# Optimization experiments

Measured on AMD Instinct MI355X. Metric: run time of the kernel, lower is better.

The kernel has to match this reference:

```python
import jax, jax.numpy as jnp
import numpy as np

N = 179  # hardcoded positional-bias size in the source module
LN_EPS = 1e-5

def _spec_attn_wghts(dtype=jnp.float32):
    i = jnp.arange(N)
    return (jnp.abs(i[None, :] - i[:, None]) / N).astype(dtype)  # [N, N]

def setup_inputs() -> dict:
    key = jax.random.key(0)
    ks = jax.random.split(key, 4)
    B, S, E = 128, 179, 1024
    x = jax.random.normal(ks[0], (B, S, E), dtype=jnp.float32)
    Wq = jax.random.normal(ks[1], (E, E), dtype=jnp.float32) * (E ** -0.5)
    Wk = jax.random.normal(ks[2], (E, E), dtype=jnp.float32) * (E ** -0.5)
    Wv = jax.random.normal(ks[3], (E, E), dtype=jnp.float32) * (E ** -0.5)
    gamma = jnp.ones((E,), dtype=jnp.float32)
    beta = jnp.zeros((E,), dtype=jnp.float32)
    return {"x": x, "Wq": Wq, "Wk": Wk, "Wv": Wv, "gamma": gamma, "beta": beta}

def reference(x, Wq, Wk, Wv, gamma, beta):
    B, S, E = x.shape
    H = 16
    D = E // H
    scale = E ** -0.5  # note: source scales by emb_size**-0.5, not head_dim
    # torch Linear(bias=False): y = x @ W.T
    q = (x @ Wq.T).reshape(B, S, H, D).transpose(0, 2, 1, 3)  # [B,H,S,D]
    k = (x @ Wk.T).reshape(B, S, H, D).transpose(0, 2, 1, 3)
    v = (x @ Wv.T).reshape(B, S, H, D).transpose(0, 2, 1, 3)
    w = _spec_attn_wghts(x.dtype)  # [S,S] multiplicative positional bias
    attn = jnp.einsum('bhqd,bhkd->bhqk', q, k) * scale * w
    attn = jax.nn.softmax(attn, axis=-1)
    out = jnp.einsum('bhqk,bhkd->bhqd', attn, v)  # [B,H,S,D]
    out = out.transpose(0, 2, 1, 3).reshape(B, S, E)
    # LayerNorm over last dim
    mu = jnp.mean(out, axis=-1, keepdims=True)
    var = jnp.var(out, axis=-1, keepdims=True)
    out = (out - mu) * jax.lax.rsqrt(var + LN_EPS) * gamma + beta
    return out
```

## Files before the change

### kernel.cpp

```cpp
#include <hip/hip_runtime.h>
#include <hip/hip_bf16.h>
#include <math.h>

#define S_LEN  179
#define M_TOT  22912
#define S_PAD  192

typedef __attribute__((ext_vector_type(8))) short short8;
typedef __attribute__((ext_vector_type(4))) float f32x4;
typedef __attribute__((ext_vector_type(4))) unsigned short ushort4v;

__device__ inline unsigned short f2bf(float f) {
    union { float f; unsigned int i; } v; v.f = f;
    unsigned int x = v.i;
    unsigned int r = x + 0x7FFFu + ((x >> 16) & 1u);
    return (unsigned short)(r >> 16);
}
__device__ inline int imin(int a, int b) { return a < b ? a : b; }

__device__ inline void gl_lds16(const unsigned short* g, unsigned short* l) {
    __builtin_amdgcn_global_load_lds(
        (const __attribute__((address_space(1))) unsigned int*)g,
        (__attribute__((address_space(3))) unsigned int*)l, 16, 0, 0);
}


#define XQUADS 5865472
#define WQUADS 262144
__global__ __launch_bounds__(256) void cast_all(
    const float* __restrict__ x,
    const float* __restrict__ Wq,
    const float* __restrict__ Wk,
    const float* __restrict__ Wv,
    unsigned short* __restrict__ xb,
    unsigned short* __restrict__ wb)
{
    const int t = blockIdx.x * 256 + threadIdx.x;
    const float* src;
    unsigned short* dst;
    size_t off;
    if (t < XQUADS) {
        src = x; dst = xb; off = (size_t)t * 4;
    } else {
        const int u = t - XQUADS;
        const int mat = u / WQUADS;
        src = (mat == 0) ? Wq : (mat == 1 ? Wk : Wv);
        dst = wb + (size_t)mat * 1048576;
        off = (size_t)(u - mat * WQUADS) * 4;
    }
    const float4 f = *(const float4*)(src + off);
    ushort4v o;
    o[0] = f2bf(f.x); o[1] = f2bf(f.y); o[2] = f2bf(f.z); o[3] = f2bf(f.w);
    *(ushort4v*)(dst + off) = o;
}

__global__ __launch_bounds__(256) void qkv_gemm2(
    const unsigned short* __restrict__ xb,
    const unsigned short* __restrict__ wb,
    unsigned short* __restrict__ qb,
    unsigned short* __restrict__ kb,
    unsigned short* __restrict__ vT)
{
    __shared__ __align__(16) unsigned short As[128 * 64];
    __shared__ __align__(16) unsigned short Bs[128 * 64];

    const int zi = blockIdx.z;
    const unsigned short* W = wb + (size_t)zi * 1048576;
    const int m0 = blockIdx.x * 128;
    const int n0 = blockIdx.y * 128;
    const int tid  = threadIdx.x;
    const int wave = tid >> 6;
    const int lane = tid & 63;
    const int ln   = lane & 15;
    const int quad = lane >> 4;
    const int wm = (wave & 1) * 64;
    const int wn = (wave >> 1) * 64;

    const int srow  = tid >> 3;
    const int pchunk = tid & 7;
    const int lchunk = pchunk ^ (srow & 7);
    const unsigned short* ag = xb + (size_t)(m0 + srow) * 1024 + lchunk * 8;
    const unsigned short* bg = W  + (size_t)(n0 + srow) * 1024 + lchunk * 8;
    unsigned short* al = &As[srow * 64 + pchunk * 8];
    unsigned short* bl = &Bs[srow * 64 + pchunk * 8];

    f32x4 acc[4][4];
    #pragma unroll
    for (int i = 0; i < 4; ++i)
        #pragma unroll
        for (int j = 0; j < 4; ++j) acc[i][j] = (f32x4){0.f, 0.f, 0.f, 0.f};

    for (int kt = 0; kt < 16; ++kt) {
        const int k0 = kt * 64;
        #pragma unroll
        for (int i = 0; i < 4; ++i) {
            gl_lds16(ag + (size_t)i * 32 * 1024 + k0, al + i * 32 * 64);
            gl_lds16(bg + (size_t)i * 32 * 1024 + k0, bl + i * 32 * 64);
        }
        __syncthreads();
        #pragma unroll
        for (int kh = 0; kh < 2; ++kh) {
            short8 af[4], bf_[4];
            #pragma unroll
            for (int mi = 0; mi < 4; ++mi) {
                const int row = wm + mi * 16 + ln;
                const int pc  = (kh * 4 + quad) ^ (ln & 7);
                af[mi] = *(const short8*)&As[row * 64 + pc * 8];
            }
            #pragma unroll
            for (int ni = 0; ni < 4; ++ni) {
                const int row = wn + ni * 16 + ln;
                const int pc  = (kh * 4 + quad) ^ (ln & 7);
                bf_[ni] = *(const short8*)&Bs[row * 64 + pc * 8];
            }
            #pragma unroll
            for (int mi = 0; mi < 4; ++mi)
                #pragma unroll
                for (int ni = 0; ni < 4; ++ni)
                    acc[mi][ni] = __builtin_amdgcn_mfma_f32_16x16x32_bf16(af[mi], bf_[ni], acc[mi][ni], 0, 0, 0);
        }
        __syncthreads();
    }

    if (zi < 2) {
        unsigned short* out = (zi == 0) ? qb : kb;
        #pragma unroll
        for (int mi = 0; mi < 4; ++mi)
            #pragma unroll
            for (int ni = 0; ni < 4; ++ni) {
                const int col = n0 + wn + ni * 16 + ln;
                #pragma unroll
                for (int r = 0; r < 4; ++r) {
                    const int row = m0 + wm + mi * 16 + quad * 4 + r;
                    out[(size_t)row * 1024 + col] = f2bf(acc[mi][ni][r]);
                }
            }
    } else {
        #pragma unroll
        for (int mi = 0; mi < 4; ++mi)
            #pragma unroll
            for (int ni = 0; ni < 4; ++ni) {
                const int col = n0 + wn + ni * 16 + ln;
                const int h = col >> 6, d = col & 63;
                #pragma unroll
                for (int r = 0; r < 4; ++r) {
                    const int row = m0 + wm + mi * 16 + quad * 4 + r;
                    const int b = row / 179;
                    const int s = row - b * 179;
                    vT[(((size_t)b * 16 + h) * 64 + d) * S_PAD + s] = f2bf(acc[mi][ni][r]);
                }
            }
    }
}

__global__ void vt_pad_zero(unsigned short* __restrict__ vT)
{
    const int idx = blockIdx.x * 256 + threadIdx.x;
    const int row = idx >> 4;
    const int j   = idx & 15;
    if (j < 13)
        vT[(size_t)row * S_PAD + 179 + j] = 0;
}

__global__ __launch_bounds__(256) void attn2(
    const unsigned short* __restrict__ qb,
    const unsigned short* __restrict__ kb,
    const unsigned short* __restrict__ vT,
    float* __restrict__ out)
{
    __shared__ unsigned short pbuf[4][16][208];

    const int bh   = blockIdx.x;
    const int b    = bh >> 4;
    const int h    = bh & 15;
    const int qt   = blockIdx.y;
    const int wave = threadIdx.x >> 6;
    const int lane = threadIdx.x & 63;
    const int ln   = lane & 15;
    const int quad = lane >> 4;
    const int qs   = qt * 64 + wave * 16;
    const size_t mrow = (size_t)b * S_LEN;

    f32x4 sc[12];
    #pragma unroll
    for (int i = 0; i < 12; ++i) sc[i] = (f32x4){0.f, 0.f, 0.f, 0.f};

    const int qoff = imin(qs + ln, S_LEN - 1);
    const unsigned short* qrow = qb + (mrow + qoff) * 1024 + h * 64 + quad * 8;
    const short8 a0 = *(const short8*)(qrow);
    const short8 a1 = *(const short8*)(qrow + 32);
    #pragma unroll
    for (int nt = 0; nt < 12; ++nt) {
        const int koffr = imin(nt * 16 + ln, S_LEN - 1);
        const unsigned short* krow = kb + (mrow + koffr) * 1024 + h * 64 + quad * 8;
        const short8 b0 = *(const short8*)(krow);
        const short8 b1 = *(const short8*)(krow + 32);
        sc[nt] = __builtin_amdgcn_mfma_f32_16x16x32_bf16(a0, b0, sc[nt], 0, 0, 0);
        sc[nt] = __builtin_amdgcn_mfma_f32_16x16x32_bf16(a1, b1, sc[nt], 0, 0, 0);
    }

    const float CW = 1.0f / (179.0f * 32.0f);
    float mx[4] = {-INFINITY, -INFINITY, -INFINITY, -INFINITY};
    #pragma unroll
    for (int nt = 0; nt < 12; ++nt) {
        const int k = nt * 16 + ln;
        #pragma unroll
        for (int r = 0; r < 4; ++r) {
            const int q = qs + quad * 4 + r;
            float v;
            if (k < S_LEN) {
                int d = q - k; if (d < 0) d = -d;
                v = sc[nt][r] * ((float)d * CW);
            } else {
                v = -INFINITY;
            }
            sc[nt][r] = v;
            mx[r] = fmaxf(mx[r], v);
        }
    }
    #pragma unroll
    for (int r = 0; r < 4; ++r) {
        float m = mx[r];
        m = fmaxf(m, __shfl_xor(m, 1));
        m = fmaxf(m, __shfl_xor(m, 2));
        m = fmaxf(m, __shfl_xor(m, 4));
        m = fmaxf(m, __shfl_xor(m, 8));
        mx[r] = m;
    }
    float sum[4] = {0.f, 0.f, 0.f, 0.f};
    #pragma unroll
    for (int nt = 0; nt < 12; ++nt)
        #pragma unroll
        for (int r = 0; r < 4; ++r) {
            const float e = __expf(sc[nt][r] - mx[r]);
            sc[nt][r] = e;
            sum[r] += e;
        }
    #pragma unroll
    for (int r = 0; r < 4; ++r) {
        float s = sum[r];
        s += __shfl_xor(s, 1);
        s += __shfl_xor(s, 2);
        s += __shfl_xor(s, 4);
        s += __shfl_xor(s, 8);
        sum[r] = 1.0f / s;
    }

    #pragma unroll
    for (int nt = 0; nt < 12; ++nt)
        #pragma unroll
        for (int r = 0; r < 4; ++r)
            pbuf[wave][quad * 4 + r][nt * 16 + ln] = f2bf(sc[nt][r] * sum[r]);

    f32x4 o[4];
    #pragma unroll
    for (int i = 0; i < 4; ++i) o[i] = (f32x4){0.f, 0.f, 0.f, 0.f};
    const unsigned short* vbase = vT + (size_t)bh * 64 * S_PAD;
    #pragma unroll
    for (int kt = 0; kt < 6; ++kt) {
        const short8 pa = *(const short8*)&pbuf[wave][ln][kt * 32 + quad * 8];
        #pragma unroll
        for (int n2 = 0; n2 < 4; ++n2) {
            const short8 vb = *(const short8*)(vbase + (size_t)(n2 * 16 + ln) * S_PAD + kt * 32 + quad * 8);
            o[n2] = __builtin_amdgcn_mfma_f32_16x16x32_bf16(pa, vb, o[n2], 0, 0, 0);
        }
    }

    #pragma unroll
    for (int n2 = 0; n2 < 4; ++n2) {
        const int col = h * 64 + n2 * 16 + ln;
        #pragma unroll
        for (int r = 0; r < 4; ++r) {
            const int q = qs + quad * 4 + r;
            if (q < S_LEN)
                out[(mrow + q) * 1024 + col] = o[n2][r];
        }
    }
}

__device__ inline short8 ldcvt8(const float* p) {
    const float4 f0 = *(const float4*)p;
    const float4 f1 = *(const float4*)(p + 4);
    short8 r;
    r[0] = (short)(__float_as_uint(f0.x) >> 16); r[1] = (short)(__float_as_uint(f0.y) >> 16);
    r[2] = (short)(__float_as_uint(f0.z) >> 16); r[3] = (short)(__float_as_uint(f0.w) >> 16);
    r[4] = (short)(__float_as_uint(f1.x) >> 16); r[5] = (short)(__float_as_uint(f1.y) >> 16);
    r[6] = (short)(__float_as_uint(f1.z) >> 16); r[7] = (short)(__float_as_uint(f1.w) >> 16);
    return r;
}

__device__ inline void proj48(const float* __restrict__ xb,
                              const float* __restrict__ Wm,
                              int h, int wave, int quad, int ln,
                              f32x4 (&acc)[3][4])
{
    #pragma unroll
    for (int t = 0; t < 3; ++t)
        #pragma unroll
        for (int nt = 0; nt < 4; ++nt) acc[t][nt] = (f32x4){0.f, 0.f, 0.f, 0.f};

    const float* wr[4];
    #pragma unroll
    for (int nt = 0; nt < 4; ++nt)
        wr[nt] = Wm + (size_t)(h * 64 + nt * 16 + ln) * 1024;
    const float* xr[3];
    #pragma unroll
    for (int t = 0; t < 3; ++t) {
        int q = wave * 16 + 64 * t + ln;
        if (q > S_LEN - 1) q = S_LEN - 1;
        xr[t] = xb + (size_t)q * 1024;
    }
    for (int kk = 0; kk < 32; ++kk) {
        const int k0 = kk * 32 + quad * 8;
        short8 bfr[4];
        #pragma unroll
        for (int nt = 0; nt < 4; ++nt) bfr[nt] = ldcvt8(wr[nt] + k0);
        short8 af[3];
        #pragma unroll
        for (int t = 0; t < 3; ++t) af[t] = ldcvt8(xr[t] + k0);
        #pragma unroll
        for (int t = 0; t < 3; ++t)
            #pragma unroll
            for (int nt = 0; nt < 4; ++nt)
                acc[t][nt] = __builtin_amdgcn_mfma_f32_16x16x32_bf16(af[t], bfr[nt], acc[t][nt], 0, 0, 0);
    }
}

__global__ __launch_bounds__(256) void fused_attn(
    const float* __restrict__ x,
    const float* __restrict__ Wq,
    const float* __restrict__ Wk,
    const float* __restrict__ Wv,
    float* __restrict__ out)
{
    __shared__ __align__(16) unsigned short Ks[192 * 72];
    __shared__ __align__(16) unsigned short Vt[64 * 200];
    __shared__ __align__(16) unsigned short WScr[4][16 * 72];

    const int bh   = blockIdx.x;
    const int b    = bh >> 4;
    const int h    = bh & 15;
    const int wave = threadIdx.x >> 6;
    const int lane = threadIdx.x & 63;
    const int ln   = lane & 15;
    const int quad = lane >> 4;
    const float* xb = x + (size_t)b * S_LEN * 1024;

    f32x4 acc[3][4];
    short8 qa[3][2];
    unsigned short* scr = &WScr[wave][0];

    proj48(xb, Wq, h, wave, quad, ln, acc);
    #pragma unroll
    for (int t = 0; t < 3; ++t) {
        #pragma unroll
        for (int nt = 0; nt < 4; ++nt)
            #pragma unroll
            for (int r = 0; r < 4; ++r)
                scr[(quad * 4 + r) * 72 + nt * 16 + ln] = f2bf(acc[t][nt][r]);
        qa[t][0] = *(const short8*)&scr[ln * 72 + quad * 8];
        qa[t][1] = *(const short8*)&scr[ln * 72 + 32 + quad * 8];
    }

    proj48(xb, Wk, h, wave, quad, ln, acc);
    #pragma unroll
    for (int t = 0; t < 3; ++t)
        #pragma unroll
        for (int nt = 0; nt < 4; ++nt)
            #pragma unroll
            for (int r = 0; r < 4; ++r)
                Ks[(wave * 16 + 64 * t + quad * 4 + r) * 72 + nt * 16 + ln] = f2bf(acc[t][nt][r]);

    proj48(xb, Wv, h, wave, quad, ln, acc);
    #pragma unroll
    for (int t = 0; t < 3; ++t)
        #pragma unroll
        for (int nt = 0; nt < 4; ++nt)
            #pragma unroll
            for (int r = 0; r < 4; ++r)
                Vt[(nt * 16 + ln) * 200 + wave * 16 + 64 * t + quad * 4 + r] = f2bf(acc[t][nt][r]);

    __syncthreads();

    const float CW = 1.0f / (179.0f * 32.0f);
    #pragma unroll 1
    for (int t = 0; t < 3; ++t) {
        const int q0 = wave * 16 + 64 * t;

        f32x4 sc[12];
        #pragma unroll
        for (int i = 0; i < 12; ++i) sc[i] = (f32x4){0.f, 0.f, 0.f, 0.f};
        #pragma unroll
        for (int nt = 0; nt < 12; ++nt) {
            const short8 kb0 = *(const short8*)&Ks[(nt * 16 + ln) * 72 + quad * 8];
            const short8 kb1 = *(const short8*)&Ks[(nt * 16 + ln) * 72 + 32 + quad * 8];
            sc[nt] = __builtin_amdgcn_mfma_f32_16x16x32_bf16(qa[t][0], kb0, sc[nt], 0, 0, 0);
            sc[nt] = __builtin_amdgcn_mfma_f32_16x16x32_bf16(qa[t][1], kb1, sc[nt], 0, 0, 0);
        }

        float mx[4] = {-INFINITY, -INFINITY, -INFINITY, -INFINITY};
        #pragma unroll
        for (int nt = 0; nt < 12; ++nt) {
            const int k = nt * 16 + ln;
            #pragma unroll
            for (int r = 0; r < 4; ++r) {
                const int q = q0 + quad * 4 + r;
                float v;
                if (k < S_LEN) {
                    int d = q - k; if (d < 0) d = -d;
                    v = sc[nt][r] * ((float)d * CW);
                } else {
                    v = -INFINITY;
                }
                sc[nt][r] = v;
                mx[r] = fmaxf(mx[r], v);
            }
        }
        #pragma unroll
        for (int r = 0; r < 4; ++r) {
            float m = mx[r];
            m = fmaxf(m, __shfl_xor(m, 1));
            m = fmaxf(m, __shfl_xor(m, 2));
            m = fmaxf(m, __shfl_xor(m, 4));
            m = fmaxf(m, __shfl_xor(m, 8));
            mx[r] = m;
        }
        float sum[4] = {0.f, 0.f, 0.f, 0.f};
        #pragma unroll
        for (int nt = 0; nt < 12; ++nt)
            #pragma unroll
            for (int r = 0; r < 4; ++r) {
                const float e = __expf(sc[nt][r] - mx[r]);
                sc[nt][r] = e;
                sum[r] += e;
            }
        #pragma unroll
        for (int r = 0; r < 4; ++r) {
            float s = sum[r];
            s += __shfl_xor(s, 1);
            s += __shfl_xor(s, 2);
            s += __shfl_xor(s, 4);
            s += __shfl_xor(s, 8);
            sum[r] = 1.0f / s;
        }

        f32x4 o[4];
        #pragma unroll
        for (int i = 0; i < 4; ++i) o[i] = (f32x4){0.f, 0.f, 0.f, 0.f};
        #pragma unroll
        for (int kt = 0; kt < 6; ++kt) {
            #pragma unroll
            for (int c = 0; c < 2; ++c) {
                const int nt = kt * 2 + c;
                #pragma unroll
                for (int r = 0; r < 4; ++r)
                    scr[(quad * 4 + r) * 40 + c * 16 + ln] = f2bf(sc[nt][r] * sum[r]);
            }
            const short8 pa = *(const short8*)&scr[ln * 40 + quad * 8];
            #pragma unroll
            for (int n2 = 0; n2 < 4; ++n2) {
                const short8 vb = *(const short8*)&Vt[(n2 * 16 + ln) * 200 + kt * 32 + quad * 8];
                o[n2] = __builtin_amdgcn_mfma_f32_16x16x32_bf16(pa, vb, o[n2], 0, 0, 0);
            }
        }

        #pragma unroll
        for (int n2 = 0; n2 < 4; ++n2) {
            const int col = h * 64 + n2 * 16 + ln;
            #pragma unroll
            for (int r = 0; r < 4; ++r) {
                const int q = q0 + quad * 4 + r;
                if (q < S_LEN)
                    out[((size_t)b * S_LEN + q) * 1024 + col] = o[n2][r];
            }
        }
    }
}

__global__ __launch_bounds__(256) void ln_kernel(
    float* __restrict__ io,
    const float* __restrict__ g,
    const float* __restrict__ be)
{
    __shared__ float red[8];
    const int row = blockIdx.x;
    const int tid = threadIdx.x;
    float* p = io + (size_t)row * 1024 + tid * 4;

    const float4 u = *(const float4*)p;
    float v[4] = {u.x, u.y, u.z, u.w};
    float sum = 0.f, sq = 0.f;
    #pragma unroll
    for (int j = 0; j < 4; ++j) {
        sum += v[j];
        sq  += v[j] * v[j];
    }
    #pragma unroll
    for (int off = 1; off < 64; off <<= 1) {
        sum += __shfl_xor(sum, off);
        sq  += __shfl_xor(sq, off);
    }
    const int wv = tid >> 6, lane = tid & 63;
    if (lane == 0) { red[wv] = sum; red[4 + wv] = sq; }
    __syncthreads();
    sum = red[0] + red[1] + red[2] + red[3];
    sq  = red[4] + red[5] + red[6] + red[7];
    const float mean = sum * (1.0f / 1024.0f);
    const float var  = fmaxf(sq * (1.0f / 1024.0f) - mean * mean, 0.0f);
    const float inv  = rsqrtf(var + 1e-5f);
    const float4 gg = *(const float4*)(g + tid * 4);
    const float4 bb = *(const float4*)(be + tid * 4);
    float4 o;
    o.x = (v[0] - mean) * inv * gg.x + bb.x;
    o.y = (v[1] - mean) * inv * gg.y + bb.y;
    o.z = (v[2] - mean) * inv * gg.z + bb.z;
    o.w = (v[3] - mean) * inv * gg.w + bb.w;
    *(float4*)p = o;
}

extern "C" void kernel_launch(void* const* d_in, const int* in_sizes, int n_in,
                              void* d_out, int out_size, void* d_ws, size_t ws_size,
                              hipStream_t stream)
{
    const float* x     = (const float*)d_in[0];
    const float* Wq    = (const float*)d_in[1];
    const float* Wk    = (const float*)d_in[2];
    const float* Wv    = (const float*)d_in[3];
    const float* gamma = (const float*)d_in[4];
    const float* beta  = (const float*)d_in[5];
    float* out = (float*)d_out;

    const size_t XB  = (size_t)M_TOT * 1024 * 2;
    const size_t WBB = (size_t)3 * 1048576 * 2;
    const size_t QBB = XB, KBB = XB;
    const size_t VTB = (size_t)2048 * 64 * S_PAD * 2;
    const size_t NEED = XB + WBB + QBB + KBB + VTB;

    if (ws_size >= NEED) {
        char* ws = (char*)d_ws;
        unsigned short* xb = (unsigned short*)(ws);
        unsigned short* wb = (unsigned short*)(ws + XB);
        unsigned short* qb = (unsigned short*)(ws + XB + WBB);
        unsigned short* kb = (unsigned short*)(ws + XB + WBB + QBB);
        unsigned short* vT = (unsigned short*)(ws + XB + WBB + QBB + KBB);

        cast_all<<<25984, 256, 0, stream>>>(x, Wq, Wk, Wv, xb, wb);
        qkv_gemm2<<<dim3(179, 8, 3), 256, 0, stream>>>(xb, wb, qb, kb, vT);
        vt_pad_zero<<<8192, 256, 0, stream>>>(vT);
        attn2<<<dim3(2048, 3), 256, 0, stream>>>(qb, kb, vT, out);
        ln_kernel<<<M_TOT, 256, 0, stream>>>(out, gamma, beta);
    } else {
        fused_attn<<<2048, 256, 0, stream>>>(x, Wq, Wk, Wv, out);
        ln_kernel<<<M_TOT, 256, 0, stream>>>(out, gamma, beta);
    }
}
```

Baseline: 592.1 us.

## Stage K and V in LDS once per head and loop over query tiles

The attention kernel now launches one block per (batch, head) instead of three. Each block loads that head's K and V^T into padded shared memory once, then loops over three 64-row query tiles and reads K and V from LDS rather than global memory. The probability staging buffer shrinks to a per-wave 16x32 scratch that is filled one k-chunk at a time before each PV MFMA. This removes redundant global loads of K and V across query tiles, at the cost of fewer blocks (less parallelism), more LDS per block, and serialised query tiles within each block.

```diff
diff --git a/kernel.cpp b/kernel.cpp
--- a/kernel.cpp
+++ b/kernel.cpp
@@ -162,118 +162,147 @@
         vT[(size_t)row * S_PAD + 179 + j] = 0;
 }
 
-__global__ __launch_bounds__(256) void attn2(
+__global__ __launch_bounds__(256) void attn3(
     const unsigned short* __restrict__ qb,
     const unsigned short* __restrict__ kb,
     const unsigned short* __restrict__ vT,
     float* __restrict__ out)
 {
-    __shared__ unsigned short pbuf[4][16][208];
+    __shared__ __align__(16) unsigned short Ks[192 * 72];
+    __shared__ __align__(16) unsigned short Vs[64 * 200];
+    __shared__ __align__(16) unsigned short Ps[4][16 * 40];
 
     const int bh   = blockIdx.x;
     const int b    = bh >> 4;
     const int h    = bh & 15;
-    const int qt   = blockIdx.y;
-    const int wave = threadIdx.x >> 6;
-    const int lane = threadIdx.x & 63;
+    const int tid  = threadIdx.x;
+    const int wave = tid >> 6;
+    const int lane = tid & 63;
     const int ln   = lane & 15;
     const int quad = lane >> 4;
-    const int qs   = qt * 64 + wave * 16;
     const size_t mrow = (size_t)b * S_LEN;
-
-    f32x4 sc[12];
-    #pragma unroll
-    for (int i = 0; i < 12; ++i) sc[i] = (f32x4){0.f, 0.f, 0.f, 0.f};
-
-    const int qoff = imin(qs + ln, S_LEN - 1);
-    const unsigned short* qrow = qb + (mrow + qoff) * 1024 + h * 64 + quad * 8;
-    const short8 a0 = *(const short8*)(qrow);
-    const short8 a1 = *(const short8*)(qrow + 32);
-    #pragma unroll
-    for (int nt = 0; nt < 12; ++nt) {
-        const int koffr = imin(nt * 16 + ln, S_LEN - 1);
-        const unsigned short* krow = kb + (mrow + koffr) * 1024 + h * 64 + quad * 8;
-        const short8 b0 = *(const short8*)(krow);
-        const short8 b1 = *(const short8*)(krow + 32);
-        sc[nt] = __builtin_amdgcn_mfma_f32_16x16x32_bf16(a0, b0, sc[nt], 0, 0, 0);
-        sc[nt] = __builtin_amdgcn_mfma_f32_16x16x32_bf16(a1, b1, sc[nt], 0, 0, 0);
-    }
+    unsigned short* scr = &Ps[wave][0];
+
+    {
+        const int r = tid >> 3;
+        const int c = tid & 7;
+        #pragma unroll
+        for (int it = 0; it < 6; ++it) {
+            const int row = it * 32 + r;
+            const int src = imin(row, S_LEN - 1);
+            const short8 v = *(const short8*)(kb + (mrow + src) * 1024 + h * 64 + c * 8);
+            *(short8*)&Ks[row * 72 + c * 8] = v;
+        }
+    }
+    {
+        const unsigned short* vbase = vT + (size_t)bh * 64 * S_PAD;
+        #pragma unroll
+        for (int it = 0; it < 6; ++it) {
+            const int idx = it * 256 + tid;
+            const int d = idx / 24;
+            const int c = idx - d * 24;
+            const short8 v = *(const short8*)(vbase + (size_t)d * S_PAD + c * 8);
+            *(short8*)&Vs[d * 200 + c * 8] = v;
+        }
+    }
+    __syncthreads();
 
     const float CW = 1.0f / (179.0f * 32.0f);
-    float mx[4] = {-INFINITY, -INFINITY, -INFINITY, -INFINITY};
-    #pragma unroll
-    for (int nt = 0; nt < 12; ++nt) {
-        const int k = nt * 16 + ln;
+    #pragma unroll 1
+    for (int t = 0; t < 3; ++t) {
+        const int qs = t * 64 + wave * 16;
+
+        const int qoff = imin(qs + ln, S_LEN - 1);
+        const unsigned short* qrow = qb + (mrow + qoff) * 1024 + h * 64 + quad * 8;
+        const short8 a0 = *(const short8*)(qrow);
+        const short8 a1 = *(const short8*)(qrow + 32);
+
+        f32x4 sc[12];
+        #pragma unroll
+        for (int i = 0; i < 12; ++i) sc[i] = (f32x4){0.f, 0.f, 0.f, 0.f};
+        #pragma unroll
+        for (int nt = 0; nt < 12; ++nt) {
+            const short8 kb0 = *(const short8*)&Ks[(nt * 16 + ln) * 72 + quad * 8];
+            const short8 kb1 = *(const short8*)&Ks[(nt * 16 + ln) * 72 + 32 + quad * 8];
+            sc[nt] = __builtin_amdgcn_mfma_f32_16x16x32_bf16(a0, kb0, sc[nt], 0, 0, 0);
+            sc[nt] = __builtin_amdgcn_mfma_f32_16x16x32_bf16(a1, kb1, sc[nt], 0, 0, 0);
+        }
+
+        float mx[4] = {-INFINITY, -INFINITY, -INFINITY, -INFINITY};
+        #pragma unroll
+        for (int nt = 0; nt < 12; ++nt) {
+            const int k = nt * 16 + ln;
+            #pragma unroll
+            for (int r = 0; r < 4; ++r) {
+                const int q = qs + quad * 4 + r;
+                float v;
+                if (k < S_LEN) {
+                    int d = q - k; if (d < 0) d = -d;
+                    v = sc[nt][r] * ((float)d * CW);
+                } else {
+                    v = -INFINITY;
+                }
+                sc[nt][r] = v;
+                mx[r] = fmaxf(mx[r], v);
+            }
+        }
         #pragma unroll
         for (int r = 0; r < 4; ++r) {
-            const int q = qs + quad * 4 + r;
-            float v;
-            if (k < S_LEN) {
-                int d = q - k; if (d < 0) d = -d;
-                v = sc[nt][r] * ((float)d * CW);
-            } else {
-                v = -INFINITY;
-            }
-            sc[nt][r] = v;
-            mx[r] = fmaxf(mx[r], v);
-        }
-    }
-    #pragma unroll
-    for (int r = 0; r < 4; ++r) {
-        float m = mx[r];
-        m = fmaxf(m, __shfl_xor(m, 1));
-        m = fmaxf(m, __shfl_xor(m, 2));
-        m = fmaxf(m, __shfl_xor(m, 4));
-        m = fmaxf(m, __shfl_xor(m, 8));
-        mx[r] = m;
-    }
-    float sum[4] = {0.f, 0.f, 0.f, 0.f};
-    #pragma unroll
-    for (int nt = 0; nt < 12; ++nt)
+            float m = mx[r];
+            m = fmaxf(m, __shfl_xor(m, 1));
+            m = fmaxf(m, __shfl_xor(m, 2));
+            m = fmaxf(m, __shfl_xor(m, 4));
+            m = fmaxf(m, __shfl_xor(m, 8));
+            mx[r] = m;
+        }
+        float sum[4] = {0.f, 0.f, 0.f, 0.f};
+        #pragma unroll
+        for (int nt = 0; nt < 12; ++nt)
+            #pragma unroll
+            for (int r = 0; r < 4; ++r) {
+                const float e = __expf(sc[nt][r] - mx[r]);
+                sc[nt][r] = e;
+                sum[r] += e;
+            }
         #pragma unroll
         for (int r = 0; r < 4; ++r) {
-            const float e = __expf(sc[nt][r] - mx[r]);
-            sc[nt][r] = e;
-            sum[r] += e;
-        }
-    #pragma unroll
-    for (int r = 0; r < 4; ++r) {
-        float s = sum[r];
-        s += __shfl_xor(s, 1);
-        s += __shfl_xor(s, 2);
-        s += __shfl_xor(s, 4);
-        s += __shfl_xor(s, 8);
-        sum[r] = 1.0f / s;
-    }
-
-    #pragma unroll
-    for (int nt = 0; nt < 12; ++nt)
-        #pragma unroll
-        for (int r = 0; r < 4; ++r)
-            pbuf[wave][quad * 4 + r][nt * 16 + ln] = f2bf(sc[nt][r] * sum[r]);
-
-    f32x4 o[4];
-    #pragma unroll
-    for (int i = 0; i < 4; ++i) o[i] = (f32x4){0.f, 0.f, 0.f, 0.f};
-    const unsigned short* vbase = vT + (size_t)bh * 64 * S_PAD;
-    #pragma unroll
-    for (int kt = 0; kt < 6; ++kt) {
-        const short8 pa = *(const short8*)&pbuf[wave][ln][kt * 32 + quad * 8];
+            float s = sum[r];
+            s += __shfl_xor(s, 1);
+            s += __shfl_xor(s, 2);
+            s += __shfl_xor(s, 4);
+            s += __shfl_xor(s, 8);
+            sum[r] = 1.0f / s;
+        }
+
+        f32x4 o[4];
+        #pragma unroll
+        for (int i = 0; i < 4; ++i) o[i] = (f32x4){0.f, 0.f, 0.f, 0.f};
+        #pragma unroll
+        for (int kt = 0; kt < 6; ++kt) {
+            #pragma unroll
+            for (int c = 0; c < 2; ++c) {
+                const int nt = kt * 2 + c;
+                #pragma unroll
+                for (int r = 0; r < 4; ++r)
+                    scr[(quad * 4 + r) * 40 + c * 16 + ln] = f2bf(sc[nt][r] * sum[r]);
+            }
+            const short8 pa = *(const short8*)&scr[ln * 40 + quad * 8];
+            #pragma unroll
+            for (int n2 = 0; n2 < 4; ++n2) {
+                const short8 vb = *(const short8*)&Vs[(n2 * 16 + ln) * 200 + kt * 32 + quad * 8];
+                o[n2] = __builtin_amdgcn_mfma_f32_16x16x32_bf16(pa, vb, o[n2], 0, 0, 0);
+            }
+        }
+
         #pragma unroll
         for (int n2 = 0; n2 < 4; ++n2) {
-            const short8 vb = *(const short8*)(vbase + (size_t)(n2 * 16 + ln) * S_PAD + kt * 32 + quad * 8);
-            o[n2] = __builtin_amdgcn_mfma_f32_16x16x32_bf16(pa, vb, o[n2], 0, 0, 0);
-        }
-    }
-
-    #pragma unroll
-    for (int n2 = 0; n2 < 4; ++n2) {
-        const int col = h * 64 + n2 * 16 + ln;
-        #pragma unroll
-        for (int r = 0; r < 4; ++r) {
-            const int q = qs + quad * 4 + r;
-            if (q < S_LEN)
-                out[(mrow + q) * 1024 + col] = o[n2][r];
+            const int col = h * 64 + n2 * 16 + ln;
+            #pragma unroll
+            for (int r = 0; r < 4; ++r) {
+                const int q = qs + quad * 4 + r;
+                if (q < S_LEN)
+                    out[(mrow + q) * 1024 + col] = o[n2][r];
+            }
         }
     }
 }
@@ -547,7 +576,7 @@
         cast_all<<<25984, 256, 0, stream>>>(x, Wq, Wk, Wv, xb, wb);
         qkv_gemm2<<<dim3(179, 8, 3), 256, 0, stream>>>(xb, wb, qb, kb, vT);
         vt_pad_zero<<<8192, 256, 0, stream>>>(vT);
-        attn2<<<dim3(2048, 3), 256, 0, stream>>>(qb, kb, vT, out);
+        attn3<<<2048, 256, 0, stream>>>(qb, kb, vT, out);
         ln_kernel<<<M_TOT, 256, 0, stream>>>(out, gamma, beta);
     } else {
         fused_attn<<<2048, 256, 0, stream>>>(x, Wq, Wk, Wv, out);
```

Result: faster. 511.0 us (-13.7%).
